# Kernel optimization log

Measured on AMD Instinct MI355X. Metric: run time of the kernel, lower is better.

The kernel has to match this reference:

```python
import jax, jax.numpy as jnp
import numpy as np

H, HD, D = 16, 64, 1024
SCALE = HD ** -0.5
TEMP = 1.0
EPS = 1e-5

def setup_inputs() -> dict:
    key = jax.random.key(0)
    ks = jax.random.split(key, 10)
    B, N = 2, 2048
    lim = 1.0 / np.sqrt(D)
    def lin(k, out_d, in_d):
        k1, k2 = jax.random.split(k)
        W = jax.random.uniform(k1, (out_d, in_d), jnp.float32, -lim, lim)
        b = jax.random.uniform(k2, (out_d,), jnp.float32, -lim, lim)
        return W, b
    Wq, bq = lin(ks[0], H * HD, D)
    Wk, bk = lin(ks[1], H * HD, D)
    Wv, bv = lin(ks[2], H * HD, D)
    Wo, bo = lin(ks[3], D, H * HD)
    return {
        "x": jax.random.normal(ks[4], (B, N, D), jnp.float32),
        "adaptive_scale": jnp.ones((H,), jnp.float32),
        "Wq": Wq, "bq": bq, "Wk": Wk, "bk": bk, "Wv": Wv, "bv": bv,
        "Wo": Wo, "bo": bo,
        "gamma": jnp.ones((D,), jnp.float32),
        "beta": jnp.zeros((D,), jnp.float32),
    }

def reference(x, adaptive_scale, Wq, bq, Wk, bk, Wv, bv, Wo, bo, gamma, beta):
    B, N, _ = x.shape
    # self-attention: context = x
    Q = (x @ Wq.T + bq).reshape(B, N, H, HD)
    K = (x @ Wk.T + bk).reshape(B, N, H, HD)
    V = (x @ Wv.T + bv).reshape(B, N, H, HD)
    # per-head adaptive scale folded into scores (matches naive QK^T * scale / temp)
    scores = jnp.einsum('bnhd,bmhd->bhnm', Q, K)
    scores = scores * (SCALE * adaptive_scale)[None, :, None, None] / TEMP
    w = jax.nn.softmax(scores, axis=-1)  # [B,H,N,N]
    attn = jnp.einsum('bhnm,bmhd->bnhd', w, V).reshape(B, N, H * HD)
    y = x + (attn @ Wo.T + bo)
    mu = jnp.mean(y, axis=-1, keepdims=True)
    var = jnp.var(y, axis=-1, keepdims=True)
    return (y - mu) / jnp.sqrt(var + EPS) * gamma + beta
```

## Files before the change

### kernel.cpp

```cpp
#include <hip/hip_runtime.h>
#include <hip/hip_bf16.h>

using bf16 = __hip_bfloat16;
typedef __attribute__((ext_vector_type(8))) short short8;
typedef __attribute__((ext_vector_type(4))) float f32x4;

#define MFMA16(a, b, c) __builtin_amdgcn_mfma_f32_16x16x32_bf16((a), (b), (c), 0, 0, 0)

__device__ inline void async16(bf16* lds, const bf16* g) {
  __builtin_amdgcn_global_load_lds(
      (const __attribute__((address_space(1))) void*)g,
      (__attribute__((address_space(3))) void*)lds, 16, 0, 0);
}

__global__ __launch_bounds__(256) void cvt_all(
    const float* __restrict__ x,  const float* __restrict__ Wq,
    const float* __restrict__ Wk, const float* __restrict__ Wv,
    const float* __restrict__ Wo,
    bf16* __restrict__ xb, bf16* __restrict__ Wqb, bf16* __restrict__ Wkb,
    bf16* __restrict__ Wvb, bf16* __restrict__ Wob) {
  int i = blockIdx.x * 256 + threadIdx.x;
  const float* s; bf16* d; int off;
  if (i < 1048576)      { s = x;  d = xb;  off = i; }
  else if (i < 1310720) { s = Wq; d = Wqb; off = i - 1048576; }
  else if (i < 1572864) { s = Wk; d = Wkb; off = i - 1310720; }
  else if (i < 1835008) { s = Wv; d = Wvb; off = i - 1572864; }
  else                  { s = Wo; d = Wob; off = i - 1835008; }
  float4 v = ((const float4*)s)[off];
  struct __align__(8) B4 { bf16 a, b, c, d; };
  B4 o{__float2bfloat16(v.x), __float2bfloat16(v.y),
       __float2bfloat16(v.z), __float2bfloat16(v.w)};
  *(B4*)&d[(size_t)off * 4] = o;
}

__global__ __launch_bounds__(256) void gemm_qkv(
    const bf16* __restrict__ A,
    const bf16* __restrict__ Wq, const bf16* __restrict__ Wk, const bf16* __restrict__ Wv,
    const float* __restrict__ bq, const float* __restrict__ bk, const float* __restrict__ bv,
    const float* __restrict__ asc,
    bf16* __restrict__ Qb, bf16* __restrict__ Kb, bf16* __restrict__ Vtb) {
  __shared__ __align__(16) bf16 As[128 * 32];
  __shared__ __align__(16) bf16 Bs[128 * 32];

  const int tid = threadIdx.x;
  const int lane = tid & 63;
  const int w = tid >> 6;
  const int m0 = blockIdx.x * 128;
  const int region = blockIdx.y >> 3;
  const int n0loc = (blockIdx.y & 7) * 128;
  const int wm = (w >> 1) * 64;
  const int wn = (w & 1) * 64;
  const int rq = lane & 15;
  const int quad = lane >> 4;
  const int kq = quad * 8;

  const bf16* W = region == 0 ? Wq : (region == 1 ? Wk : Wv);
  const float* bias = region == 0 ? bq : (region == 1 ? bk : bv);
  bf16* C = region == 0 ? Qb : (region == 1 ? Kb : Vtb);

  f32x4 acc[4][4] = {};
  const bf16* Ag = A + (size_t)m0 * 1024;
  const bf16* Wg = W + (size_t)n0loc * 1024;

  for (int k0 = 0; k0 < 1024; k0 += 32) {
    __syncthreads();
#pragma unroll
    for (int rep = 0; rep < 2; ++rep) {
      int c = tid + rep * 256;
      int row = c >> 2;
      int ce = (c & 3) * 8;
      async16(&As[c * 8], Ag + (size_t)row * 1024 + k0 + ce);
      async16(&Bs[c * 8], Wg + (size_t)row * 1024 + k0 + ce);
    }
    __syncthreads();

    short8 a[4], b[4];
#pragma unroll
    for (int i = 0; i < 4; ++i) a[i] = *(const short8*)&As[(wm + i * 16 + rq) * 32 + kq];
#pragma unroll
    for (int j = 0; j < 4; ++j) b[j] = *(const short8*)&Bs[(wn + j * 16 + rq) * 32 + kq];
#pragma unroll
    for (int i = 0; i < 4; ++i)
#pragma unroll
      for (int j = 0; j < 4; ++j) acc[i][j] = MFMA16(a[i], b[j], acc[i][j]);
  }

  const float LOG2E = 1.44269504088896f;
#pragma unroll
  for (int i = 0; i < 4; ++i)
#pragma unroll
    for (int j = 0; j < 4; ++j)
#pragma unroll
      for (int r2 = 0; r2 < 4; ++r2) {
        int m = m0 + wm + i * 16 + quad * 4 + r2;
        int nr = n0loc + wn + j * 16 + rq;
        int bb = m >> 11, t = m & 2047, h = nr >> 6, hd = nr & 63;
        float v = acc[i][j][r2] + bias[nr];
        if (region == 0) v *= 0.125f * asc[h] * LOG2E;
        bf16 ov = __float2bfloat16(v);
        if (region < 2)
          C[(((size_t)(bb * 16 + h)) * 2048 + t) * 64 + hd] = ov;
        else
          C[(((size_t)(bb * 16 + h)) * 64 + hd) * 2048 + t] = ov;
      }
}

__global__ __launch_bounds__(256) void gemm_out(
    const bf16* __restrict__ A, const bf16* __restrict__ W,
    const float* __restrict__ bias, const float* __restrict__ R,
    float* __restrict__ Y) {
  __shared__ __align__(16) bf16 As[128 * 32];
  __shared__ __align__(16) bf16 Bs[128 * 32];

  const int tid = threadIdx.x;
  const int lane = tid & 63;
  const int w = tid >> 6;
  const int m0 = blockIdx.x * 128;
  const int n0 = blockIdx.y * 128;
  const int wm = (w >> 1) * 64;
  const int wn = (w & 1) * 64;
  const int rq = lane & 15;
  const int quad = lane >> 4;
  const int kq = quad * 8;

  f32x4 acc[4][4] = {};
  const bf16* Ag = A + (size_t)m0 * 1024;
  const bf16* Wg = W + (size_t)n0 * 1024;

  for (int k0 = 0; k0 < 1024; k0 += 32) {
    __syncthreads();
#pragma unroll
    for (int rep = 0; rep < 2; ++rep) {
      int c = tid + rep * 256;
      int row = c >> 2;
      int ce = (c & 3) * 8;
      async16(&As[c * 8], Ag + (size_t)row * 1024 + k0 + ce);
      async16(&Bs[c * 8], Wg + (size_t)row * 1024 + k0 + ce);
    }
    __syncthreads();

    short8 a[4], b[4];
#pragma unroll
    for (int i = 0; i < 4; ++i) a[i] = *(const short8*)&As[(wm + i * 16 + rq) * 32 + kq];
#pragma unroll
    for (int j = 0; j < 4; ++j) b[j] = *(const short8*)&Bs[(wn + j * 16 + rq) * 32 + kq];
#pragma unroll
    for (int i = 0; i < 4; ++i)
#pragma unroll
      for (int j = 0; j < 4; ++j) acc[i][j] = MFMA16(a[i], b[j], acc[i][j]);
  }

#pragma unroll
  for (int i = 0; i < 4; ++i)
#pragma unroll
    for (int j = 0; j < 4; ++j)
#pragma unroll
      for (int r2 = 0; r2 < 4; ++r2) {
        int m = m0 + wm + i * 16 + quad * 4 + r2;
        int n = n0 + wn + j * 16 + rq;
        Y[(size_t)m * 1024 + n] = acc[i][j][r2] + bias[n] + R[(size_t)m * 1024 + n];
      }
}

#define LP 72
__global__ __launch_bounds__(256) void attn_kernel(
    const bf16* __restrict__ Qb, const bf16* __restrict__ Kb,
    const bf16* __restrict__ Vtb, bf16* __restrict__ Ob) {
  __shared__ __align__(16) bf16 Ks[64 * 64];
  __shared__ __align__(16) bf16 Vs[64 * 64];
  __shared__ __align__(16) bf16 Ps[4][16 * LP];

  const int q0 = blockIdx.x * 64;
  const int h = blockIdx.y;
  const int b = blockIdx.z;
  const int tid = threadIdx.x;
  const int lane = tid & 63;
  const int w = tid >> 6;
  const int rq = lane & 15;
  const int quad = lane >> 4;
  const int kq = quad * 8;

  const size_t head = ((size_t)(b * 16 + h)) * 2048 * 64;
  const bf16* Qh = Qb + head;
  const bf16* Kh = Kb + head;
  const bf16* Vh = Vtb + head;

  const bf16* qrow = Qh + (size_t)(q0 + w * 16 + rq) * 64;
  short8 aq0 = *(const short8*)&qrow[kq];
  short8 aq1 = *(const short8*)&qrow[kq + 32];

  short8 ones;
#pragma unroll
  for (int i = 0; i < 8; ++i) ones[i] = (short)0x3F80;

  const int srow = lane >> 3;
  const int sws = ((lane & 7) ^ srow) * 8;
  const int c0 = (quad ^ (rq & 7)) * 8;
  const int c1 = c0 ^ 32;

  f32x4 accO[4] = {};
  f32x4 lacc = {};

  for (int kt = 0; kt < 32; ++kt) {
    __syncthreads();
#pragma unroll
    for (int t = 0; t < 2; ++t) {
      int rb = w * 16 + t * 8;
      int row = rb + srow;
      async16(&Ks[rb * 64 + lane * 8], Kh + (size_t)(kt * 64 + row) * 64 + sws);
      async16(&Vs[rb * 64 + lane * 8], Vh + (size_t)row * 2048 + kt * 64 + sws);
    }
    __syncthreads();

    f32x4 S[4] = {};
#pragma unroll
    for (int j = 0; j < 4; ++j) {
      short8 bk0 = *(const short8*)&Ks[(j * 16 + rq) * 64 + c0];
      short8 bk1 = *(const short8*)&Ks[(j * 16 + rq) * 64 + c1];
      S[j] = MFMA16(aq0, bk0, S[j]);
      S[j] = MFMA16(aq1, bk1, S[j]);
    }

#pragma unroll
    for (int r = 0; r < 4; ++r)
#pragma unroll
      for (int j = 0; j < 4; ++j)
        Ps[w][(quad * 4 + r) * LP + j * 16 + rq] = __float2bfloat16(exp2f(S[j][r]));

    short8 ap0 = *(const short8*)&Ps[w][rq * LP + kq];
    short8 ap1 = *(const short8*)&Ps[w][rq * LP + kq + 32];
#pragma unroll
    for (int dt = 0; dt < 4; ++dt) {
      short8 bv0 = *(const short8*)&Vs[(dt * 16 + rq) * 64 + c0];
      short8 bv1 = *(const short8*)&Vs[(dt * 16 + rq) * 64 + c1];
      accO[dt] = MFMA16(ap0, bv0, accO[dt]);
      accO[dt] = MFMA16(ap1, bv1, accO[dt]);
    }
    lacc = MFMA16(ap0, ones, lacc);
    lacc = MFMA16(ap1, ones, lacc);
  }

  float rl[4];
#pragma unroll
  for (int r = 0; r < 4; ++r) rl[r] = 1.f / lacc[r];
#pragma unroll
  for (int dt = 0; dt < 4; ++dt)
#pragma unroll
    for (int r = 0; r < 4; ++r) {
      int t = q0 + w * 16 + quad * 4 + r;
      int d = dt * 16 + rq;
      Ob[((size_t)(b * 2048 + t)) * 1024 + h * 64 + d] =
          __float2bfloat16(accO[dt][r] * rl[r]);
    }
}

__global__ __launch_bounds__(256) void ln_kernel(
    const float* __restrict__ Y, const float* __restrict__ gamma,
    const float* __restrict__ beta, float* __restrict__ out) {
  const int row = blockIdx.x;
  const int tid = threadIdx.x;
  const int lane = tid & 63;
  const int w = tid >> 6;
  const float* y = Y + (size_t)row * 1024;

  float4 v = *(const float4*)&y[tid * 4];
  float s = v.x + v.y + v.z + v.w;
  float ss = v.x * v.x + v.y * v.y + v.z * v.z + v.w * v.w;
#pragma unroll
  for (int msk = 1; msk < 64; msk <<= 1) {
    s += __shfl_xor(s, msk);
    ss += __shfl_xor(ss, msk);
  }
  __shared__ float red[2][4];
  if (lane == 0) { red[0][w] = s; red[1][w] = ss; }
  __syncthreads();
  s = red[0][0] + red[0][1] + red[0][2] + red[0][3];
  ss = red[1][0] + red[1][1] + red[1][2] + red[1][3];
  float mean = s * (1.f / 1024.f);
  float var = ss * (1.f / 1024.f) - mean * mean;
  float rstd = rsqrtf(var + 1e-5f);
  float4 g = *(const float4*)&gamma[tid * 4];
  float4 bt = *(const float4*)&beta[tid * 4];
  float4 o;
  o.x = (v.x - mean) * rstd * g.x + bt.x;
  o.y = (v.y - mean) * rstd * g.y + bt.y;
  o.z = (v.z - mean) * rstd * g.z + bt.z;
  o.w = (v.w - mean) * rstd * g.w + bt.w;
  *(float4*)&out[(size_t)row * 1024 + tid * 4] = o;
}

extern "C" void kernel_launch(void* const* d_in, const int* in_sizes, int n_in,
                              void* d_out, int out_size, void* d_ws, size_t ws_size,
                              hipStream_t stream) {
  const float* x     = (const float*)d_in[0];
  const float* asc   = (const float*)d_in[1];
  const float* Wq    = (const float*)d_in[2];
  const float* bq    = (const float*)d_in[3];
  const float* Wk    = (const float*)d_in[4];
  const float* bk    = (const float*)d_in[5];
  const float* Wv    = (const float*)d_in[6];
  const float* bv    = (const float*)d_in[7];
  const float* Wo    = (const float*)d_in[8];
  const float* bo    = (const float*)d_in[9];
  const float* gamma = (const float*)d_in[10];
  const float* beta  = (const float*)d_in[11];
  float* out = (float*)d_out;

  char* ws = (char*)d_ws;
  const size_t MB = 1024 * 1024;
  bf16* Qb   = (bf16*)(ws);
  bf16* Kb   = (bf16*)(ws + 8 * MB);
  bf16* Vtb  = (bf16*)(ws + 16 * MB);
  bf16* attn = (bf16*)(ws + 24 * MB);
  bf16* xb   = (bf16*)(ws + 32 * MB);
  bf16* Wqb  = (bf16*)(ws + 40 * MB);
  bf16* Wkb  = (bf16*)(ws + 42 * MB);
  bf16* Wvb  = (bf16*)(ws + 44 * MB);
  bf16* Wob  = (bf16*)(ws + 46 * MB);
  float* y   = (float*)(ws);

  dim3 bb(256);

  cvt_all<<<dim3(8192), bb, 0, stream>>>(x, Wq, Wk, Wv, Wo, xb, Wqb, Wkb, Wvb, Wob);
  gemm_qkv<<<dim3(32, 24), bb, 0, stream>>>(xb, Wqb, Wkb, Wvb, bq, bk, bv, asc, Qb, Kb, Vtb);
  attn_kernel<<<dim3(32, 16, 2), bb, 0, stream>>>(Qb, Kb, Vtb, attn);
  gemm_out<<<dim3(32, 8), bb, 0, stream>>>(attn, Wob, bo, x, y);
  ln_kernel<<<dim3(4096), bb, 0, stream>>>(y, gamma, beta, out);
}
```

Before: 241.4 us.

## Process two 16-row query tiles per wave in attention to reuse K/V tiles

Each attention block now covers 128 query rows instead of 64. Each wave computes two 16-row query sub-tiles against the same K and V tiles in LDS, and the grid shrinks to match. The intent is to halve K/V global loads, LDS staging and barriers per query row, and to raise MFMA density per loaded fragment. In exchange, register use grows, a launch-bounds hint is added, and fewer blocks are launched, which lowers parallelism on a large GPU.

```diff
diff --git a/kernel.cpp b/kernel.cpp
--- a/kernel.cpp
+++ b/kernel.cpp
@@ -163,14 +163,14 @@
 }
 
 #define LP 72
-__global__ __launch_bounds__(256) void attn_kernel(
+__global__ __launch_bounds__(256, 3) void attn_kernel(
     const bf16* __restrict__ Qb, const bf16* __restrict__ Kb,
     const bf16* __restrict__ Vtb, bf16* __restrict__ Ob) {
   __shared__ __align__(16) bf16 Ks[64 * 64];
   __shared__ __align__(16) bf16 Vs[64 * 64];
-  __shared__ __align__(16) bf16 Ps[4][16 * LP];
-
-  const int q0 = blockIdx.x * 64;
+  __shared__ __align__(16) bf16 Ps[4][32 * LP];
+
+  const int q0 = blockIdx.x * 128;
   const int h = blockIdx.y;
   const int b = blockIdx.z;
   const int tid = threadIdx.x;
@@ -185,9 +185,13 @@
   const bf16* Kh = Kb + head;
   const bf16* Vh = Vtb + head;
 
-  const bf16* qrow = Qh + (size_t)(q0 + w * 16 + rq) * 64;
-  short8 aq0 = *(const short8*)&qrow[kq];
-  short8 aq1 = *(const short8*)&qrow[kq + 32];
+  short8 aq[2][2];
+#pragma unroll
+  for (int s = 0; s < 2; ++s) {
+    const bf16* qrow = Qh + (size_t)(q0 + w * 32 + s * 16 + rq) * 64;
+    aq[s][0] = *(const short8*)&qrow[kq];
+    aq[s][1] = *(const short8*)&qrow[kq + 32];
+  }
 
   short8 ones;
 #pragma unroll
@@ -198,8 +202,8 @@
   const int c0 = (quad ^ (rq & 7)) * 8;
   const int c1 = c0 ^ 32;
 
-  f32x4 accO[4] = {};
-  f32x4 lacc = {};
+  f32x4 accO[2][4] = {};
+  f32x4 lacc[2] = {};
 
   for (int kt = 0; kt < 32; ++kt) {
     __syncthreads();
@@ -212,46 +216,65 @@
     }
     __syncthreads();
 
-    f32x4 S[4] = {};
+    f32x4 S[2][4] = {};
 #pragma unroll
     for (int j = 0; j < 4; ++j) {
       short8 bk0 = *(const short8*)&Ks[(j * 16 + rq) * 64 + c0];
       short8 bk1 = *(const short8*)&Ks[(j * 16 + rq) * 64 + c1];
-      S[j] = MFMA16(aq0, bk0, S[j]);
-      S[j] = MFMA16(aq1, bk1, S[j]);
-    }
-
-#pragma unroll
-    for (int r = 0; r < 4; ++r)
-#pragma unroll
-      for (int j = 0; j < 4; ++j)
-        Ps[w][(quad * 4 + r) * LP + j * 16 + rq] = __float2bfloat16(exp2f(S[j][r]));
-
-    short8 ap0 = *(const short8*)&Ps[w][rq * LP + kq];
-    short8 ap1 = *(const short8*)&Ps[w][rq * LP + kq + 32];
+      S[0][j] = MFMA16(aq[0][0], bk0, S[0][j]);
+      S[0][j] = MFMA16(aq[0][1], bk1, S[0][j]);
+      S[1][j] = MFMA16(aq[1][0], bk0, S[1][j]);
+      S[1][j] = MFMA16(aq[1][1], bk1, S[1][j]);
+    }
+
+#pragma unroll
+    for (int s = 0; s < 2; ++s)
+#pragma unroll
+      for (int r = 0; r < 4; ++r)
+#pragma unroll
+        for (int j = 0; j < 4; ++j)
+          Ps[w][(s * 16 + quad * 4 + r) * LP + j * 16 + rq] =
+              __float2bfloat16(exp2f(S[s][j][r]));
+
+    short8 ap[2][2];
+#pragma unroll
+    for (int s = 0; s < 2; ++s) {
+      ap[s][0] = *(const short8*)&Ps[w][(s * 16 + rq) * LP + kq];
+      ap[s][1] = *(const short8*)&Ps[w][(s * 16 + rq) * LP + kq + 32];
+    }
+
 #pragma unroll
     for (int dt = 0; dt < 4; ++dt) {
       short8 bv0 = *(const short8*)&Vs[(dt * 16 + rq) * 64 + c0];
       short8 bv1 = *(const short8*)&Vs[(dt * 16 + rq) * 64 + c1];
-      accO[dt] = MFMA16(ap0, bv0, accO[dt]);
-      accO[dt] = MFMA16(ap1, bv1, accO[dt]);
-    }
-    lacc = MFMA16(ap0, ones, lacc);
-    lacc = MFMA16(ap1, ones, lacc);
-  }
-
-  float rl[4];
-#pragma unroll
-  for (int r = 0; r < 4; ++r) rl[r] = 1.f / lacc[r];
-#pragma unroll
-  for (int dt = 0; dt < 4; ++dt)
-#pragma unroll
-    for (int r = 0; r < 4; ++r) {
-      int t = q0 + w * 16 + quad * 4 + r;
-      int d = dt * 16 + rq;
-      Ob[((size_t)(b * 2048 + t)) * 1024 + h * 64 + d] =
-          __float2bfloat16(accO[dt][r] * rl[r]);
-    }
+#pragma unroll
+      for (int s = 0; s < 2; ++s) {
+        accO[s][dt] = MFMA16(ap[s][0], bv0, accO[s][dt]);
+        accO[s][dt] = MFMA16(ap[s][1], bv1, accO[s][dt]);
+      }
+    }
+#pragma unroll
+    for (int s = 0; s < 2; ++s) {
+      lacc[s] = MFMA16(ap[s][0], ones, lacc[s]);
+      lacc[s] = MFMA16(ap[s][1], ones, lacc[s]);
+    }
+  }
+
+#pragma unroll
+  for (int s = 0; s < 2; ++s) {
+    float rl[4];
+#pragma unroll
+    for (int r = 0; r < 4; ++r) rl[r] = 1.f / lacc[s][r];
+#pragma unroll
+    for (int dt = 0; dt < 4; ++dt)
+#pragma unroll
+      for (int r = 0; r < 4; ++r) {
+        int t = q0 + w * 32 + s * 16 + quad * 4 + r;
+        int d = dt * 16 + rq;
+        Ob[((size_t)(b * 2048 + t)) * 1024 + h * 64 + d] =
+            __float2bfloat16(accO[s][dt][r] * rl[r]);
+      }
+  }
 }
 
 __global__ __launch_bounds__(256) void ln_kernel(
@@ -323,7 +346,7 @@
 
   cvt_all<<<dim3(8192), bb, 0, stream>>>(x, Wq, Wk, Wv, Wo, xb, Wqb, Wkb, Wvb, Wob);
   gemm_qkv<<<dim3(32, 24), bb, 0, stream>>>(xb, Wqb, Wkb, Wvb, bq, bk, bv, asc, Qb, Kb, Vtb);
-  attn_kernel<<<dim3(32, 16, 2), bb, 0, stream>>>(Qb, Kb, Vtb, attn);
+  attn_kernel<<<dim3(16, 16, 2), bb, 0, stream>>>(Qb, Kb, Vtb, attn);
   gemm_out<<<dim3(32, 8), bb, 0, stream>>>(attn, Wob, bo, x, y);
   ln_kernel<<<dim3(4096), bb, 0, stream>>>(y, gamma, beta, out);
 }
```

Result: faster. 235.8 us (-2.3%).
